# Performance work log

Hardware: AMD Instinct MI355X
Metric: run time of the kernel (lower is better)

The kernel has to match this reference:

```python
import jax, jax.numpy as jnp
import numpy as np

TEMPERATURE = 32.0  # sqrt(d_model=1024)

def setup_inputs() -> dict:
    key = jax.random.key(0)
    kq, kk, kv = jax.random.split(key, 3)
    B, H, S, D = 2, 16, 2048, 64
    q = jax.random.normal(kq, (B, H, S, D), dtype=jnp.float32)
    k = jax.random.normal(kk, (B, H, S, D), dtype=jnp.float32)
    v = jax.random.normal(kv, (B, H, S, D), dtype=jnp.float32)
    mask = jnp.ones((B, 1, 1, S), dtype=jnp.int32)  # key-padding mask, 1 = keep
    return {"q": q, "k": k, "v": v, "mask": mask}

def reference(q, k, v, mask):
    # scores: [B,H,S,S]
    scores = jnp.einsum('bhqd,bhkd->bhqk', q / TEMPERATURE, k)
    scores = jnp.where(mask == 0, jnp.float32(-1e9), scores)
    attention = jax.nn.softmax(scores, axis=-1)
    # dropout is identity at inference (module's nn.Dropout in eval mode)
    output = jnp.einsum('bhqk,bhkd->bhqd', attention, v)
    return (output, attention)
```

## Files before the change

kernel.cpp:

```cpp
#include <hip/hip_runtime.h>
#include <hip/hip_bf16.h>


#define S_LEN 2048
#define D_DIM 64
#define BM 64
#define BN 64
#define NT (S_LEN / BN)
#define LDP 72
#define LDF 68
#define BH_N 32

typedef __attribute__((ext_vector_type(8))) short bf16x8;
typedef __attribute__((ext_vector_type(4))) float f32x4;

__device__ __forceinline__ unsigned pack_bf16(float a, float b) {
    union { __hip_bfloat162 h; unsigned u; } cv;
    cv.h = __float22bfloat162_rn(make_float2(a, b));
    return cv.u;
}
__device__ __forceinline__ unsigned short bf1(float x) {
    union { __hip_bfloat16 h; unsigned short u; } cv;
    cv.h = __float2bfloat16(x);
    return cv.u;
}

__global__ __launch_bounds__(256)
void conv_k(const float* __restrict__ Kg, unsigned short* __restrict__ Kw) {
    size_t i = (size_t)(blockIdx.x * 256 + threadIdx.x) * 8;
    const float4 v0 = *(const float4*)(Kg + i);
    const float4 v1 = *(const float4*)(Kg + i + 4);
    uint4 o;
    o.x = pack_bf16(v0.x, v0.y);
    o.y = pack_bf16(v0.z, v0.w);
    o.z = pack_bf16(v1.x, v1.y);
    o.w = pack_bf16(v1.z, v1.w);
    *(uint4*)(Kw + i) = o;
}

__global__ __launch_bounds__(256)
void conv_vt(const float* __restrict__ Vg, unsigned short* __restrict__ Vtw) {
    const int bh = blockIdx.y;
    const int d  = threadIdx.x & 63;
    const int kq = threadIdx.x >> 6;
    const int key0 = blockIdx.x * 32 + kq * 8;
    const float* Vb = Vg + ((size_t)bh * S_LEN + key0) * D_DIM + d;
    float f[8];
    #pragma unroll
    for (int i = 0; i < 8; ++i) f[i] = Vb[i * D_DIM];
    uint4 o;
    o.x = pack_bf16(f[0], f[1]);
    o.y = pack_bf16(f[2], f[3]);
    o.z = pack_bf16(f[4], f[5]);
    o.w = pack_bf16(f[6], f[7]);
    *(uint4*)(Vtw + ((size_t)bh * D_DIM + d) * S_LEN + key0) = o;
}

template <int PRE>
__global__ __launch_bounds__(256, 4)
void attn_kernel(const float* __restrict__ Qg, const float* __restrict__ Kg,
                 const float* __restrict__ Vg, const int* __restrict__ Mg,
                 const unsigned short* __restrict__ Kw,
                 const unsigned short* __restrict__ Vtw,
                 float* __restrict__ Og, float* __restrict__ Ag) {
    __shared__ unsigned short Ks[BN * LDP];
    __shared__ unsigned short QV[D_DIM * LDP];
    __shared__ float Pf[BM * LDF];
    __shared__ int maskS[BN];

    const int tid  = threadIdx.x;
    const int w    = tid >> 6;
    const int lane = tid & 63;
    const int l15  = lane & 15;
    const int quad = lane >> 4;

    const int qt = blockIdx.x;
    const int bh = blockIdx.y;
    const int b  = bh >> 4;
    const int q0 = qt * BM;
    const int qrow = w * 16 + l15;

    const float* Qb = Qg + ((size_t)bh * S_LEN + q0) * D_DIM;
    const int*   Mb = Mg + (size_t)b * S_LEN;
    float* Ob = Og + ((size_t)bh * S_LEN + q0) * D_DIM;
    float* Ab = Ag + ((size_t)bh * S_LEN + q0) * (size_t)S_LEN;

    {
        const float sc = 0.04508422f;
        #pragma unroll
        for (int i = 0; i < 4; ++i) {
            int f = tid + i * 256;
            int row = f >> 4, c4 = f & 15;
            const float4 v = *(const float4*)(Qb + row * D_DIM + c4 * 4);
            *(uint2*)(&QV[row * LDP + c4 * 4]) =
                make_uint2(pack_bf16(v.x * sc, v.y * sc), pack_bf16(v.z * sc, v.w * sc));
        }
    }
    __syncthreads();

    bf16x8 aq[2];
    #pragma unroll
    for (int ks = 0; ks < 2; ++ks)
        aq[ks] = *(const bf16x8*)(&QV[qrow * LDP + ks * 32 + quad * 8]);

    auto stage_k = [&](int key0) {
        if constexpr (PRE) {
            const unsigned short* Kt = Kw + (size_t)bh * S_LEN * D_DIM + (size_t)key0 * D_DIM;
            #pragma unroll
            for (int i = 0; i < 2; ++i) {
                int idx = tid + i * 256;
                int row = idx >> 3, c = idx & 7;
                uint4 vv = *(const uint4*)(Kt + row * D_DIM + c * 8);
                *(uint4*)(&Ks[row * LDP + c * 8]) = vv;
            }
        } else {
            const float* Kb = Kg + ((size_t)bh * S_LEN + key0) * D_DIM;
            #pragma unroll
            for (int i = 0; i < 4; ++i) {
                int f = tid + i * 256;
                int row = f >> 4, c4 = f & 15;
                const float4 v = *(const float4*)(Kb + row * D_DIM + c4 * 4);
                *(uint2*)(&Ks[row * LDP + c4 * 4]) =
                    make_uint2(pack_bf16(v.x, v.y), pack_bf16(v.z, v.w));
            }
        }
    };

    float lsum = 0.f;

    for (int kt = 0; kt < NT; ++kt) {
        const int key0 = kt * BN;
        stage_k(key0);
        if (tid < BN) maskS[tid] = Mb[key0 + tid];
        __syncthreads();

        #pragma unroll
        for (int cb = 0; cb < 4; ++cb) {
            f32x4 acc = {0.f, 0.f, 0.f, 0.f};
            #pragma unroll
            for (int ks = 0; ks < 2; ++ks) {
                bf16x8 bk = *(const bf16x8*)(&Ks[(cb * 16 + l15) * LDP + ks * 32 + quad * 8]);
                acc = __builtin_amdgcn_mfma_f32_16x16x32_bf16(bk, aq[ks], acc, 0, 0, 0);
            }
            const int4 m4 = *(const int4*)(&maskS[cb * 16 + quad * 4]);
            float e0 = m4.x ? __builtin_exp2f(acc[0]) : 0.f;
            float e1 = m4.y ? __builtin_exp2f(acc[1]) : 0.f;
            float e2 = m4.z ? __builtin_exp2f(acc[2]) : 0.f;
            float e3 = m4.w ? __builtin_exp2f(acc[3]) : 0.f;
            lsum += (e0 + e1) + (e2 + e3);
        }
        __syncthreads();
    }

    lsum += __shfl_xor(lsum, 16);
    lsum += __shfl_xor(lsum, 32);
    const float linv = 1.0f / lsum;

    f32x4 oacc[4];
    #pragma unroll
    for (int db = 0; db < 4; ++db) oacc[db] = (f32x4){0.f, 0.f, 0.f, 0.f};

    for (int kt = 0; kt < NT; ++kt) {
        const int key0 = kt * BN;
        stage_k(key0);
        if constexpr (PRE) {
            const unsigned short* Vt = Vtw + (size_t)bh * D_DIM * S_LEN + key0;
            #pragma unroll
            for (int i = 0; i < 2; ++i) {
                int idx = tid + i * 256;
                int d = idx >> 3, c = idx & 7;
                uint4 vv = *(const uint4*)(Vt + (size_t)d * S_LEN + c * 8);
                *(uint4*)(&QV[d * LDP + c * 8]) = vv;
            }
        } else {
            int key = tid & 63, g = tid >> 6;
            #pragma unroll
            for (int i = 0; i < 4; ++i) {
                int d0 = (g * 4 + i) * 4;
                const float4 v = *(const float4*)(Vg + ((size_t)bh * S_LEN + key0 + key) * D_DIM + d0);
                QV[(d0 + 0) * LDP + key] = bf1(v.x);
                QV[(d0 + 1) * LDP + key] = bf1(v.y);
                QV[(d0 + 2) * LDP + key] = bf1(v.z);
                QV[(d0 + 3) * LDP + key] = bf1(v.w);
            }
        }
        if (tid < BN) maskS[tid] = Mb[key0 + tid];
        __syncthreads();

        #pragma unroll
        for (int cb = 0; cb < 4; ++cb) {
            f32x4 acc = {0.f, 0.f, 0.f, 0.f};
            #pragma unroll
            for (int ks = 0; ks < 2; ++ks) {
                bf16x8 bk = *(const bf16x8*)(&Ks[(cb * 16 + l15) * LDP + ks * 32 + quad * 8]);
                acc = __builtin_amdgcn_mfma_f32_16x16x32_bf16(bk, aq[ks], acc, 0, 0, 0);
            }
            const int4 m4 = *(const int4*)(&maskS[cb * 16 + quad * 4]);
            f32x4 p;
            p[0] = (m4.x ? __builtin_exp2f(acc[0]) : 0.f) * linv;
            p[1] = (m4.y ? __builtin_exp2f(acc[1]) : 0.f) * linv;
            p[2] = (m4.z ? __builtin_exp2f(acc[2]) : 0.f) * linv;
            p[3] = (m4.w ? __builtin_exp2f(acc[3]) : 0.f) * linv;
            *(f32x4*)(&Pf[qrow * LDF + cb * 16 + quad * 4]) = p;
        }

        #pragma unroll
        for (int ks2 = 0; ks2 < 2; ++ks2) {
            const float* pr = &Pf[qrow * LDF + ks2 * 32 + quad * 8];
            f32x4 pa = *(const f32x4*)(pr);
            f32x4 pb = *(const f32x4*)(pr + 4);
            union { bf16x8 v; uint4 u; } ap;
            ap.u.x = pack_bf16(pa[0], pa[1]);
            ap.u.y = pack_bf16(pa[2], pa[3]);
            ap.u.z = pack_bf16(pb[0], pb[1]);
            ap.u.w = pack_bf16(pb[2], pb[3]);
            #pragma unroll
            for (int db = 0; db < 4; ++db) {
                bf16x8 bv = *(const bf16x8*)(&QV[(db * 16 + l15) * LDP + ks2 * 32 + quad * 8]);
                oacc[db] = __builtin_amdgcn_mfma_f32_16x16x32_bf16(bv, ap.v, oacc[db], 0, 0, 0);
            }
        }
        __syncthreads();

        #pragma unroll
        for (int i = 0; i < 4; ++i) {
            int idx = tid + i * 256;
            int row = idx >> 4, c4 = idx & 15;
            f32x4 t = *(const f32x4*)(&Pf[row * LDF + c4 * 4]);
            __builtin_nontemporal_store(
                t, (f32x4*)(Ab + (size_t)row * S_LEN + key0 + c4 * 4));
        }
    }

    #pragma unroll
    for (int db = 0; db < 4; ++db) {
        f32x4 o4 = oacc[db];
        __builtin_nontemporal_store(
            o4, (f32x4*)(Ob + (size_t)qrow * D_DIM + db * 16 + quad * 4));
    }
}

extern "C" void kernel_launch(void* const* d_in, const int* in_sizes, int n_in,
                              void* d_out, int out_size, void* d_ws, size_t ws_size,
                              hipStream_t stream) {
    const float* q = (const float*)d_in[0];
    const float* k = (const float*)d_in[1];
    const float* v = (const float*)d_in[2];
    const int* mask = (const int*)d_in[3];
    float* out = (float*)d_out;
    float* attn = out + (size_t)2 * 16 * 2048 * 64;

    const size_t kw_elems = (size_t)BH_N * S_LEN * D_DIM;
    const size_t need = 2 * kw_elems * sizeof(unsigned short);
    dim3 block(256);
    dim3 grid(S_LEN / BM, BH_N);

    if (d_ws && ws_size >= need) {
        unsigned short* Kw  = (unsigned short*)d_ws;
        unsigned short* Vtw = Kw + kw_elems;
        conv_k<<<dim3((unsigned)(kw_elems / 8 / 256)), block, 0, stream>>>(k, Kw);
        conv_vt<<<dim3(S_LEN / 32, BH_N), block, 0, stream>>>(v, Vtw);
        attn_kernel<1><<<grid, block, 0, stream>>>(q, k, v, mask, Kw, Vtw, out, attn);
    } else {
        attn_kernel<0><<<grid, block, 0, stream>>>(q, k, v, mask, nullptr, nullptr, out, attn);
    }
}
```

Measured before the change: 644.6 us.

## Load K/V MFMA operands directly from global, drop LDS staging and block barriers

```diff
diff --git a/kernel.cpp b/kernel.cpp
--- a/kernel.cpp
+++ b/kernel.cpp
@@ -8,7 +8,6 @@
 #define BN 64
 #define NT (S_LEN / BN)
 #define LDP 72
-#define LDF 68
 #define BH_N 32
 
 typedef __attribute__((ext_vector_type(8))) short bf16x8;
@@ -23,6 +22,10 @@
     union { __hip_bfloat16 h; unsigned short u; } cv;
     cv.h = __float2bfloat16(x);
     return cv.u;
+}
+
+__device__ __forceinline__ float* pf_ptr(float* Pf, int row, int chunk) {
+    return Pf + row * 64 + ((chunk ^ (row & 7)) << 2);
 }
 
 __global__ __launch_bounds__(256)
@@ -56,16 +59,144 @@
     *(uint4*)(Vtw + ((size_t)bh * D_DIM + d) * S_LEN + key0) = o;
 }
 
-template <int PRE>
 __global__ __launch_bounds__(256, 4)
-void attn_kernel(const float* __restrict__ Qg, const float* __restrict__ Kg,
-                 const float* __restrict__ Vg, const int* __restrict__ Mg,
-                 const unsigned short* __restrict__ Kw,
-                 const unsigned short* __restrict__ Vtw,
-                 float* __restrict__ Og, float* __restrict__ Ag) {
+void attn_fast(const float* __restrict__ Qg, const int* __restrict__ Mg,
+               const unsigned short* __restrict__ Kw,
+               const unsigned short* __restrict__ Vtw,
+               float* __restrict__ Og, float* __restrict__ Ag) {
+    __shared__ float Pf[BM * 64];
+
+    const int tid  = threadIdx.x;
+    const int w    = tid >> 6;
+    const int lane = tid & 63;
+    const int l15  = lane & 15;
+    const int quad = lane >> 4;
+
+    const int qt = blockIdx.x;
+    const int bh = blockIdx.y;
+    const int b  = bh >> 4;
+    const int q0 = qt * BM;
+    const int qrow = w * 16 + l15;
+
+    const float* Qb = Qg + ((size_t)bh * S_LEN + q0) * D_DIM;
+    const int*   Mb = Mg + (size_t)b * S_LEN;
+    float* Ob = Og + ((size_t)bh * S_LEN + q0) * D_DIM;
+    float* Ab = Ag + ((size_t)bh * S_LEN + q0) * (size_t)S_LEN;
+
+    const unsigned short* Kb = Kw  + (size_t)bh * S_LEN * D_DIM;
+    const unsigned short* Vb = Vtw + (size_t)bh * D_DIM * S_LEN;
+
+    bf16x8 aq[2];
+    {
+        const float sc = 0.04508422f;
+        #pragma unroll
+        for (int ks = 0; ks < 2; ++ks) {
+            const float* qp = Qb + qrow * D_DIM + ks * 32 + quad * 8;
+            const float4 a = *(const float4*)(qp);
+            const float4 c = *(const float4*)(qp + 4);
+            union { bf16x8 v; uint4 u; } cv;
+            cv.u.x = pack_bf16(a.x * sc, a.y * sc);
+            cv.u.y = pack_bf16(a.z * sc, a.w * sc);
+            cv.u.z = pack_bf16(c.x * sc, c.y * sc);
+            cv.u.w = pack_bf16(c.z * sc, c.w * sc);
+            aq[ks] = cv.v;
+        }
+    }
+
+    const int koff = l15 * D_DIM + quad * 8;
+    const size_t vbase = (size_t)l15 * S_LEN + quad * 8;
+
+    float lsum = 0.f;
+    for (int kt = 0; kt < NT; ++kt) {
+        const unsigned short* Kt = Kb + (size_t)kt * BN * D_DIM + koff;
+        const int* Mt = Mb + kt * BN + quad * 4;
+        #pragma unroll
+        for (int cb = 0; cb < 4; ++cb) {
+            f32x4 acc = {0.f, 0.f, 0.f, 0.f};
+            #pragma unroll
+            for (int ks = 0; ks < 2; ++ks) {
+                bf16x8 bk = *(const bf16x8*)(Kt + cb * (16 * D_DIM) + ks * 32);
+                acc = __builtin_amdgcn_mfma_f32_16x16x32_bf16(bk, aq[ks], acc, 0, 0, 0);
+            }
+            const int4 m4 = *(const int4*)(Mt + cb * 16);
+            float e0 = m4.x ? __builtin_exp2f(acc[0]) : 0.f;
+            float e1 = m4.y ? __builtin_exp2f(acc[1]) : 0.f;
+            float e2 = m4.z ? __builtin_exp2f(acc[2]) : 0.f;
+            float e3 = m4.w ? __builtin_exp2f(acc[3]) : 0.f;
+            lsum += (e0 + e1) + (e2 + e3);
+        }
+    }
+    lsum += __shfl_xor(lsum, 16);
+    lsum += __shfl_xor(lsum, 32);
+    const float linv = 1.0f / lsum;
+
+    f32x4 oacc[4];
+    #pragma unroll
+    for (int db = 0; db < 4; ++db) oacc[db] = (f32x4){0.f, 0.f, 0.f, 0.f};
+
+    for (int kt = 0; kt < NT; ++kt) {
+        const int key0 = kt * BN;
+        const unsigned short* Kt = Kb + (size_t)key0 * D_DIM + koff;
+        const int* Mt = Mb + key0 + quad * 4;
+
+        #pragma unroll
+        for (int cb = 0; cb < 4; ++cb) {
+            f32x4 acc = {0.f, 0.f, 0.f, 0.f};
+            #pragma unroll
+            for (int ks = 0; ks < 2; ++ks) {
+                bf16x8 bk = *(const bf16x8*)(Kt + cb * (16 * D_DIM) + ks * 32);
+                acc = __builtin_amdgcn_mfma_f32_16x16x32_bf16(bk, aq[ks], acc, 0, 0, 0);
+            }
+            const int4 m4 = *(const int4*)(Mt + cb * 16);
+            f32x4 p;
+            p[0] = (m4.x ? __builtin_exp2f(acc[0]) : 0.f) * linv;
+            p[1] = (m4.y ? __builtin_exp2f(acc[1]) : 0.f) * linv;
+            p[2] = (m4.z ? __builtin_exp2f(acc[2]) : 0.f) * linv;
+            p[3] = (m4.w ? __builtin_exp2f(acc[3]) : 0.f) * linv;
+            *(f32x4*)pf_ptr(Pf, qrow, cb * 4 + quad) = p;
+        }
+
+        #pragma unroll
+        for (int ks2 = 0; ks2 < 2; ++ks2) {
+            const f32x4 pa = *(const f32x4*)pf_ptr(Pf, qrow, ks2 * 8 + quad * 2);
+            const f32x4 pb = *(const f32x4*)pf_ptr(Pf, qrow, ks2 * 8 + quad * 2 + 1);
+            union { bf16x8 v; uint4 u; } ap;
+            ap.u.x = pack_bf16(pa[0], pa[1]);
+            ap.u.y = pack_bf16(pa[2], pa[3]);
+            ap.u.z = pack_bf16(pb[0], pb[1]);
+            ap.u.w = pack_bf16(pb[2], pb[3]);
+            const unsigned short* Vt = Vb + vbase + key0 + ks2 * 32;
+            #pragma unroll
+            for (int db = 0; db < 4; ++db) {
+                bf16x8 bv = *(const bf16x8*)(Vt + (size_t)db * (16 * S_LEN));
+                oacc[db] = __builtin_amdgcn_mfma_f32_16x16x32_bf16(bv, ap.v, oacc[db], 0, 0, 0);
+            }
+        }
+
+        #pragma unroll
+        for (int i = 0; i < 4; ++i) {
+            const int row = w * 16 + i * 4 + quad;
+            f32x4 t = *(const f32x4*)pf_ptr(Pf, row, l15);
+            __builtin_nontemporal_store(
+                t, (f32x4*)(Ab + (size_t)row * S_LEN + key0 + l15 * 4));
+        }
+    }
+
+    #pragma unroll
+    for (int db = 0; db < 4; ++db) {
+        f32x4 o4 = oacc[db];
+        __builtin_nontemporal_store(
+            o4, (f32x4*)(Ob + (size_t)qrow * D_DIM + db * 16 + quad * 4));
+    }
+}
+
+__global__ __launch_bounds__(256, 4)
+void attn_fallback(const float* __restrict__ Qg, const float* __restrict__ Kg,
+                   const float* __restrict__ Vg, const int* __restrict__ Mg,
+                   float* __restrict__ Og, float* __restrict__ Ag) {
     __shared__ unsigned short Ks[BN * LDP];
     __shared__ unsigned short QV[D_DIM * LDP];
-    __shared__ float Pf[BM * LDF];
+    __shared__ float Pf[BM * 68];
     __shared__ int maskS[BN];
 
     const int tid  = threadIdx.x;
@@ -104,36 +235,23 @@
         aq[ks] = *(const bf16x8*)(&QV[qrow * LDP + ks * 32 + quad * 8]);
 
     auto stage_k = [&](int key0) {
-        if constexpr (PRE) {
-            const unsigned short* Kt = Kw + (size_t)bh * S_LEN * D_DIM + (size_t)key0 * D_DIM;
-            #pragma unroll
-            for (int i = 0; i < 2; ++i) {
-                int idx = tid + i * 256;
-                int row = idx >> 3, c = idx & 7;
-                uint4 vv = *(const uint4*)(Kt + row * D_DIM + c * 8);
-                *(uint4*)(&Ks[row * LDP + c * 8]) = vv;
-            }
-        } else {
-            const float* Kb = Kg + ((size_t)bh * S_LEN + key0) * D_DIM;
-            #pragma unroll
-            for (int i = 0; i < 4; ++i) {
-                int f = tid + i * 256;
-                int row = f >> 4, c4 = f & 15;
-                const float4 v = *(const float4*)(Kb + row * D_DIM + c4 * 4);
-                *(uint2*)(&Ks[row * LDP + c4 * 4]) =
-                    make_uint2(pack_bf16(v.x, v.y), pack_bf16(v.z, v.w));
-            }
+        const float* Kb = Kg + ((size_t)bh * S_LEN + key0) * D_DIM;
+        #pragma unroll
+        for (int i = 0; i < 4; ++i) {
+            int f = tid + i * 256;
+            int row = f >> 4, c4 = f & 15;
+            const float4 v = *(const float4*)(Kb + row * D_DIM + c4 * 4);
+            *(uint2*)(&Ks[row * LDP + c4 * 4]) =
+                make_uint2(pack_bf16(v.x, v.y), pack_bf16(v.z, v.w));
         }
     };
 
     float lsum = 0.f;
-
     for (int kt = 0; kt < NT; ++kt) {
         const int key0 = kt * BN;
         stage_k(key0);
         if (tid < BN) maskS[tid] = Mb[key0 + tid];
         __syncthreads();
-
         #pragma unroll
         for (int cb = 0; cb < 4; ++cb) {
             f32x4 acc = {0.f, 0.f, 0.f, 0.f};
@@ -151,7 +269,6 @@
         }
         __syncthreads();
     }
-
     lsum += __shfl_xor(lsum, 16);
     lsum += __shfl_xor(lsum, 32);
     const float linv = 1.0f / lsum;
@@ -163,16 +280,7 @@
     for (int kt = 0; kt < NT; ++kt) {
         const int key0 = kt * BN;
         stage_k(key0);
-        if constexpr (PRE) {
-            const unsigned short* Vt = Vtw + (size_t)bh * D_DIM * S_LEN + key0;
-            #pragma unroll
-            for (int i = 0; i < 2; ++i) {
-                int idx = tid + i * 256;
-                int d = idx >> 3, c = idx & 7;
-                uint4 vv = *(const uint4*)(Vt + (size_t)d * S_LEN + c * 8);
-                *(uint4*)(&QV[d * LDP + c * 8]) = vv;
-            }
-        } else {
+        {
             int key = tid & 63, g = tid >> 6;
             #pragma unroll
             for (int i = 0; i < 4; ++i) {
@@ -201,12 +309,11 @@
             p[1] = (m4.y ? __builtin_exp2f(acc[1]) : 0.f) * linv;
             p[2] = (m4.z ? __builtin_exp2f(acc[2]) : 0.f) * linv;
             p[3] = (m4.w ? __builtin_exp2f(acc[3]) : 0.f) * linv;
-            *(f32x4*)(&Pf[qrow * LDF + cb * 16 + quad * 4]) = p;
-        }
-
+            *(f32x4*)(&Pf[qrow * 68 + cb * 16 + quad * 4]) = p;
+        }
         #pragma unroll
         for (int ks2 = 0; ks2 < 2; ++ks2) {
-            const float* pr = &Pf[qrow * LDF + ks2 * 32 + quad * 8];
+            const float* pr = &Pf[qrow * 68 + ks2 * 32 + quad * 8];
             f32x4 pa = *(const f32x4*)(pr);
             f32x4 pb = *(const f32x4*)(pr + 4);
             union { bf16x8 v; uint4 u; } ap;
@@ -221,12 +328,11 @@
             }
         }
         __syncthreads();
-
         #pragma unroll
         for (int i = 0; i < 4; ++i) {
             int idx = tid + i * 256;
             int row = idx >> 4, c4 = idx & 15;
-            f32x4 t = *(const f32x4*)(&Pf[row * LDF + c4 * 4]);
+            f32x4 t = *(const f32x4*)(&Pf[row * 68 + c4 * 4]);
             __builtin_nontemporal_store(
                 t, (f32x4*)(Ab + (size_t)row * S_LEN + key0 + c4 * 4));
         }
@@ -260,8 +366,8 @@
         unsigned short* Vtw = Kw + kw_elems;
         conv_k<<<dim3((unsigned)(kw_elems / 8 / 256)), block, 0, stream>>>(k, Kw);
         conv_vt<<<dim3(S_LEN / 32, BH_N), block, 0, stream>>>(v, Vtw);
-        attn_kernel<1><<<grid, block, 0, stream>>>(q, k, v, mask, Kw, Vtw, out, attn);
+        attn_fast<<<grid, block, 0, stream>>>(q, mask, Kw, Vtw, out, attn);
     } else {
-        attn_kernel<0><<<grid, block, 0, stream>>>(q, k, v, mask, nullptr, nullptr, out, attn);
-    }
-}
+        attn_fallback<<<grid, block, 0, stream>>>(q, k, v, mask, out, attn);
+    }
+}
```

Result: slower. 862.1 us (+33.7%).
